# Kernel optimization log

Hardware: AMD Instinct MI355X
Metric: run time of the kernel (lower is better)

Reference implementation:

```python
import jax, jax.numpy as jnp
import numpy as np

D_MODEL, H, DH = 1024, 16, 64
S, B, LCACHE = 16, 8, 8192
W_SCALE = 0.02  # keep pre-softmax logits in a sane range


def setup_inputs() -> dict:
    key = jax.random.key(0)
    ks = jax.random.split(key, 7)
    return {
        "x": jax.random.normal(ks[0], (S, B, D_MODEL), jnp.float32),
        "cache_k": jax.random.normal(ks[1], (LCACHE, B, H, DH), jnp.float32),
        "cache_v": jax.random.normal(ks[2], (LCACHE, B, H, DH), jnp.float32),
        "Wq": jax.random.normal(ks[3], (D_MODEL, H * DH), jnp.float32) * W_SCALE,
        "Wk": jax.random.normal(ks[4], (D_MODEL, H * DH), jnp.float32) * W_SCALE,
        "Wv": jax.random.normal(ks[5], (D_MODEL, H * DH), jnp.float32) * W_SCALE,
        "Wo": jax.random.normal(ks[6], (H * DH, D_MODEL), jnp.float32) * W_SCALE,
    }


def reference(x, cache_k, cache_v, Wq, Wk, Wv, Wo):
    S, B, D = x.shape
    Lc, _, H, Dh = cache_k.shape
    # project and split heads: (S, B, H, Dh)
    q = (x @ Wq).reshape(S, B, H, Dh)
    k_new = (x @ Wk).reshape(S, B, H, Dh)
    v_new = (x @ Wv).reshape(S, B, H, Dh)
    # extend cache along time axis -> (L, B, H, Dh), L = Lc + S
    new_k = jnp.concatenate([cache_k, k_new], axis=0)
    new_v = jnp.concatenate([cache_v, v_new], axis=0)
    L = Lc + S
    scale = 1.0 / jnp.sqrt(jnp.asarray(Dh, x.dtype))
    # scores: (B, H, S, L)
    scores = jnp.einsum('sbhd,tbhd->bhst', q, new_k) * scale
    # causal: query at position Lc+s attends to key positions t <= Lc+s
    mask = jnp.arange(L)[None, :] <= (Lc + jnp.arange(S))[:, None]  # (S, L)
    scores = jnp.where(mask[None, None], scores, jnp.asarray(-1e9, scores.dtype))
    attn = jax.nn.softmax(scores, axis=-1)
    ctx = jnp.einsum('bhst,tbhd->sbhd', attn, new_v).reshape(S, B, H * Dh)
    res = ctx @ Wo  # (S, B, D)
    return res, new_k, new_v
```

## Files before the change

### kernel.cpp

```cpp
#include <hip/hip_runtime.h>
#include <hip/hip_bf16.h>

#define S 16
#define B 8
#define H 16
#define DH 64
#define D 1024
#define HD 1024
#define LC 8192
#define LMAX (LC + S)
#define NCH 32
#define CHT 256
#define TILE 32
#define NT (CHT / TILE)

typedef __attribute__((ext_vector_type(4))) float f4;
typedef __attribute__((ext_vector_type(4))) short s4v;
typedef __attribute__((ext_vector_type(8))) short s8v;

__device__ inline short bfs(float f) {
    __hip_bfloat16 h = __float2bfloat16(f);
    return __builtin_bit_cast(short, h);
}
__device__ inline s4v pack4(float a, float b, float c, float d) {
    s4v r; r[0] = bfs(a); r[1] = bfs(b); r[2] = bfs(c); r[3] = bfs(d); return r;
}

__global__ __launch_bounds__(256) void proj_qkv(const float* __restrict__ x,
        const float* __restrict__ Wq, const float* __restrict__ Wk,
        const float* __restrict__ Wv,
        float* __restrict__ q_ws, float* __restrict__ newk, float* __restrict__ newv)
{
    int bx = blockIdx.x;
    int rg  = bx / 12;
    int rem = bx % 12;
    int mat = rem >> 2, chunk = rem & 3;
    int o = chunk * 256 + threadIdx.x;
    const float* W  = (mat == 0) ? Wq : ((mat == 1) ? Wk : Wv);
    const float* xr = x + (size_t)rg * 4 * D;

    float a0 = 0.f, a1 = 0.f, a2 = 0.f, a3 = 0.f;
    #pragma unroll 16
    for (int d = 0; d < D; ++d) {
        float w = W[(size_t)d * HD + o];
        a0 += xr[d] * w;
        a1 += xr[D + d] * w;
        a2 += xr[2 * D + d] * w;
        a3 += xr[3 * D + d] * w;
    }
    float acc[4] = {a0, a1, a2, a3};
    #pragma unroll
    for (int i = 0; i < 4; ++i) {
        int row = rg * 4 + i;
        int s = row >> 3, b = row & 7;
        if (mat == 0) {
            q_ws[(size_t)row * HD + o] = acc[i];
        } else {
            float* dst = (mat == 1) ? newk : newv;
            dst[(size_t)((LC + s) * B + b) * HD + o] = acc[i];
        }
    }
}

__global__ __launch_bounds__(256) void attn_fused(const float* __restrict__ q_ws,
        const float* __restrict__ cache_k, const float* __restrict__ cache_v,
        float* __restrict__ newk, float* __restrict__ newv,
        float* __restrict__ m_part, float* __restrict__ l_part,
        float* __restrict__ pv_part)
{
    extern __shared__ char smem[];
    short* Ksp = (short*)smem;
    short* Vp  = Ksp + TILE * 256;

    int bx = blockIdx.x;
    int chunk = bx & 31;
    int hgb = bx >> 5;
    int hg = hgb & 3, b = hgb >> 2;
    int tid = threadIdx.x, l = tid & 63, wid = tid >> 6;
    int g = l >> 4, c16 = l & 15;
    int h = hg * 4 + wid;
    unsigned vbase = (unsigned)(uintptr_t)Vp + (unsigned)wid * 4160u;

    s8v qf[2];
    {
        const float* qp = q_ws + ((size_t)(c16 * B + b)) * HD + h * DH + g * 8;
        #pragma unroll
        for (int sl = 0; sl < 2; ++sl) {
            float4 qa = *(const float4*)(qp + sl * 32);
            float4 qb = *(const float4*)(qp + sl * 32 + 4);
            s8v q;
            q[0] = bfs(qa.x * 0.125f); q[1] = bfs(qa.y * 0.125f);
            q[2] = bfs(qa.z * 0.125f); q[3] = bfs(qa.w * 0.125f);
            q[4] = bfs(qb.x * 0.125f); q[5] = bfs(qb.y * 0.125f);
            q[6] = bfs(qb.z * 0.125f); q[7] = bfs(qb.w * 0.125f);
            qf[sl] = q;
        }
    }

    float m_prev = -1e30f, l_acc = 0.f;
    f4 acc[4] = {{0,0,0,0},{0,0,0,0},{0,0,0,0},{0,0,0,0}};

    int t0base = chunk * CHT;
    int sw = (c16 & 7) << 3;

    for (int it = 0; it < NT; ++it) {
        int t0 = t0base + it * TILE;
        asm volatile("s_waitcnt lgkmcnt(0)" ::: "memory");
        __builtin_amdgcn_s_barrier();
        __builtin_amdgcn_sched_barrier(0);

        #pragma unroll
        for (int gg = 0; gg < 8; ++gg) {
            int idx = tid + gg * 256;
            int rr = idx >> 6, ch = idx & 63;
            size_t off = ((size_t)(t0 + rr)) * 8192 + (size_t)b * 1024 + hg * 256 + ch * 4;
            f4 k4 = __builtin_nontemporal_load((const f4*)(cache_k + off));
            f4 v4 = __builtin_nontemporal_load((const f4*)(cache_v + off));
            __builtin_nontemporal_store(k4, (f4*)(newk + off));
            __builtin_nontemporal_store(v4, (f4*)(newv + off));
            int w = ch >> 4, cc = ch & 15;
            int kidx = rr * 256 + w * 64 + ((cc * 4) ^ ((rr & 7) << 3));
            *(s4v*)(Ksp + kidx) = pack4(k4[0], k4[1], k4[2], k4[3]);
            int vidx = w * 2080 + (cc >> 2) * 520 + (rr >> 2) * 64 + (rr & 3) * 16 + (cc & 3) * 4;
            *(s4v*)(Vp + vidx) = pack4(v4[0], v4[1], v4[2], v4[3]);
        }
        asm volatile("s_waitcnt lgkmcnt(0)" ::: "memory");
        __builtin_amdgcn_s_barrier();
        __builtin_amdgcn_sched_barrier(0);

        f4 d0 = {0,0,0,0}, d1 = {0,0,0,0};
        #pragma unroll
        for (int sl = 0; sl < 2; ++sl) {
            int col = (sl * 32 + g * 8) ^ sw;
            s8v k0 = *(const s8v*)(Ksp + c16 * 256 + wid * 64 + col);
            s8v k1 = *(const s8v*)(Ksp + (16 + c16) * 256 + wid * 64 + col);
            d0 = __builtin_amdgcn_mfma_f32_16x16x32_bf16(k0, qf[sl], d0, 0, 0, 0);
            d1 = __builtin_amdgcn_mfma_f32_16x16x32_bf16(k1, qf[sl], d1, 0, 0, 0);
        }
        float hm = fmaxf(fmaxf(fmaxf(d0[0], d0[1]), fmaxf(d0[2], d0[3])),
                         fmaxf(fmaxf(d1[0], d1[1]), fmaxf(d1[2], d1[3])));
        hm = fmaxf(hm, __shfl_xor(hm, 16));
        hm = fmaxf(hm, __shfl_xor(hm, 32));
        float mn = fmaxf(m_prev, hm);
        float sf = __expf(m_prev - mn);
        m_prev = mn;
        f4 p0, p1;
        #pragma unroll
        for (int r = 0; r < 4; ++r) { p0[r] = __expf(d0[r] - mn); p1[r] = __expf(d1[r] - mn); }
        float rs = (p0[0] + p0[1] + p0[2] + p0[3]) + (p1[0] + p1[1] + p1[2] + p1[3]);
        rs += __shfl_xor(rs, 16);
        rs += __shfl_xor(rs, 32);
        l_acc = l_acc * sf + rs;
        #pragma unroll
        for (int dd = 0; dd < 4; ++dd) acc[dd] *= sf;

        s4v pb0 = pack4(p0[0], p0[1], p0[2], p0[3]);
        s4v pb1 = pack4(p1[0], p1[1], p1[2], p1[3]);
        s4v vfr[4][2];
        #pragma unroll
        for (int dd = 0; dd < 4; ++dd) {
            #pragma unroll
            for (int hh = 0; hh < 2; ++hh) {
                unsigned adr = vbase + 2u * (unsigned)(dd * 520 + (hh * 4 + g) * 64 + c16);
                asm volatile("ds_read_b64_tr_b16 %0, %1" : "=v"(vfr[dd][hh]) : "v"(adr));
            }
        }
        asm volatile("s_waitcnt lgkmcnt(0)" ::: "memory");
        __builtin_amdgcn_sched_barrier(0);
        #pragma unroll
        for (int dd = 0; dd < 4; ++dd) {
            acc[dd] = __builtin_amdgcn_mfma_f32_16x16x16bf16_1k(vfr[dd][0], pb0, acc[dd], 0, 0, 0);
            acc[dd] = __builtin_amdgcn_mfma_f32_16x16x16bf16_1k(vfr[dd][1], pb1, acc[dd], 0, 0, 0);
        }
    }

    if (chunk == NCH - 1) {
        __syncthreads();
        #pragma unroll
        for (int q = 0; q < 4; ++q) {
            int idx = tid + q * 256;
            int rr = idx >> 6, ch = idx & 63;
            size_t off = ((size_t)(LC + rr)) * 8192 + (size_t)b * 1024 + hg * 256 + ch * 4;
            float4 k4 = *(const float4*)(newk + off);
            float4 v4 = *(const float4*)(newv + off);
            int w = ch >> 4, cc = ch & 15;
            int kidx = rr * 256 + w * 64 + ((cc * 4) ^ ((rr & 7) << 3));
            *(s4v*)(Ksp + kidx) = pack4(k4.x, k4.y, k4.z, k4.w);
            int vidx = w * 2080 + (cc >> 2) * 520 + (rr >> 2) * 64 + (rr & 3) * 16 + (cc & 3) * 4;
            *(s4v*)(Vp + vidx) = pack4(v4.x, v4.y, v4.z, v4.w);
        }
        __syncthreads();
        f4 d0 = {0,0,0,0};
        #pragma unroll
        for (int sl = 0; sl < 2; ++sl) {
            int col = (sl * 32 + g * 8) ^ sw;
            s8v k0 = *(const s8v*)(Ksp + c16 * 256 + wid * 64 + col);
            d0 = __builtin_amdgcn_mfma_f32_16x16x32_bf16(k0, qf[sl], d0, 0, 0, 0);
        }
        #pragma unroll
        for (int r = 0; r < 4; ++r)
            if (4 * g + r > c16) d0[r] = -1e30f;
        float hm = fmaxf(fmaxf(d0[0], d0[1]), fmaxf(d0[2], d0[3]));
        hm = fmaxf(hm, __shfl_xor(hm, 16));
        hm = fmaxf(hm, __shfl_xor(hm, 32));
        float mn = fmaxf(m_prev, hm);
        float sf = __expf(m_prev - mn);
        m_prev = mn;
        f4 p0;
        #pragma unroll
        for (int r = 0; r < 4; ++r) p0[r] = __expf(d0[r] - mn);
        float rs = (p0[0] + p0[1]) + (p0[2] + p0[3]);
        rs += __shfl_xor(rs, 16);
        rs += __shfl_xor(rs, 32);
        l_acc = l_acc * sf + rs;
        #pragma unroll
        for (int dd = 0; dd < 4; ++dd) acc[dd] *= sf;
        s4v pb0 = pack4(p0[0], p0[1], p0[2], p0[3]);
        s4v vfr[4];
        #pragma unroll
        for (int dd = 0; dd < 4; ++dd) {
            unsigned adr = vbase + 2u * (unsigned)(dd * 520 + g * 64 + c16);
            asm volatile("ds_read_b64_tr_b16 %0, %1" : "=v"(vfr[dd]) : "v"(adr));
        }
        asm volatile("s_waitcnt lgkmcnt(0)" ::: "memory");
        __builtin_amdgcn_sched_barrier(0);
        #pragma unroll
        for (int dd = 0; dd < 4; ++dd)
            acc[dd] = __builtin_amdgcn_mfma_f32_16x16x16bf16_1k(vfr[dd], pb0, acc[dd], 0, 0, 0);
    }

    int pi = ((b * 16 + h) * NCH) + chunk;
    #pragma unroll
    for (int dd = 0; dd < 4; ++dd)
        #pragma unroll
        for (int r = 0; r < 4; ++r)
            pv_part[((size_t)pi * 64 + dd * 16 + g * 4 + r) * 16 + c16] = acc[dd][r];
    if (l < 16) {
        m_part[pi * 16 + l] = m_prev;
        l_part[pi * 16 + l] = l_acc;
    }
}

__global__ __launch_bounds__(256) void combine(const float* __restrict__ m_part,
        const float* __restrict__ l_part, const float* __restrict__ pv_part,
        float* __restrict__ ctx)
{
    __shared__ float wexp[NCH][16];
    __shared__ float Ls[16];
    int bh = blockIdx.x;
    int h = bh & 15, b = bh >> 4;
    int tid = threadIdx.x;
    if (tid < 16) {
        int s = tid;
        float M = -1e30f;
        #pragma unroll
        for (int c = 0; c < NCH; ++c) M = fmaxf(M, m_part[(bh * NCH + c) * 16 + s]);
        float L = 0.f;
        #pragma unroll
        for (int c = 0; c < NCH; ++c) {
            float e = __expf(m_part[(bh * NCH + c) * 16 + s] - M);
            wexp[c][s] = e;
            L += e * l_part[(bh * NCH + c) * 16 + s];
        }
        Ls[s] = L;
    }
    __syncthreads();
    #pragma unroll
    for (int k = 0; k < 4; ++k) {
        int idx = tid + k * 256;
        int d = idx >> 4, s = idx & 15;
        float v = 0.f;
        #pragma unroll
        for (int c = 0; c < NCH; ++c)
            v += wexp[c][s] * pv_part[((size_t)(bh * NCH + c) * 64 + d) * 16 + s];
        ctx[((size_t)(s * B + b)) * HD + h * DH + d] = v / Ls[s];
    }
}

__global__ __launch_bounds__(256) void proj_o(const float* __restrict__ ctx,
                                              const float* __restrict__ Wo,
                                              float* __restrict__ res)
{
    int bx = blockIdx.x;
    int rg = bx >> 2, chunk = bx & 3;
    int o = chunk * 256 + threadIdx.x;
    const float* cr = ctx + (size_t)rg * 4 * HD;

    float a0 = 0.f, a1 = 0.f, a2 = 0.f, a3 = 0.f;
    #pragma unroll 16
    for (int d = 0; d < HD; ++d) {
        float w = Wo[(size_t)d * D + o];
        a0 += cr[d] * w;
        a1 += cr[HD + d] * w;
        a2 += cr[2 * HD + d] * w;
        a3 += cr[3 * HD + d] * w;
    }
    res[(size_t)(rg * 4 + 0) * D + o] = a0;
    res[(size_t)(rg * 4 + 1) * D + o] = a1;
    res[(size_t)(rg * 4 + 2) * D + o] = a2;
    res[(size_t)(rg * 4 + 3) * D + o] = a3;
}

extern "C" void kernel_launch(void* const* d_in, const int* in_sizes, int n_in,
                              void* d_out, int out_size, void* d_ws, size_t ws_size,
                              hipStream_t stream)
{
    const float* x  = (const float*)d_in[0];
    const float* ck = (const float*)d_in[1];
    const float* cv = (const float*)d_in[2];
    const float* Wq = (const float*)d_in[3];
    const float* Wk = (const float*)d_in[4];
    const float* Wv = (const float*)d_in[5];
    const float* Wo = (const float*)d_in[6];

    float* out  = (float*)d_out;
    float* res  = out;
    float* newk = out + (size_t)S * B * D;
    float* newv = newk + (size_t)LMAX * B * H * DH;

    float* q_ws    = (float*)d_ws;
    float* ctx     = q_ws + (size_t)S * B * HD;
    float* m_part  = ctx + (size_t)S * B * HD;
    float* l_part  = m_part + (size_t)B * H * NCH * S;
    float* pv_part = l_part + (size_t)B * H * NCH * S;

    size_t smem = (size_t)TILE * 256 * 2 + 4 * 2080 * 2;

    hipLaunchKernelGGL(proj_qkv, dim3(32 * 12), dim3(256), 0, stream,
                       x, Wq, Wk, Wv, q_ws, newk, newv);
    hipLaunchKernelGGL(attn_fused, dim3(B * 4 * NCH), dim3(256), smem, stream,
                       q_ws, ck, cv, newk, newv, m_part, l_part, pv_part);
    hipLaunchKernelGGL(combine, dim3(B * H), dim3(256), 0, stream,
                       m_part, l_part, pv_part, ctx);
    hipLaunchKernelGGL(proj_o, dim3(32 * 4), dim3(256), 0, stream,
                       ctx, Wo, res);
}
```

Before: 358.7 us.

## Register double-buffer KV cache loads and fuse combine with output projection

The attention kernel now prefetches the next tile of K/V cache into registers while the current tile is written to the output cache and staged to LDS. The tile shrinks to 16 rows to keep the register footprint small, and launch bounds request higher occupancy. The combine and Wo-projection kernels are merged: each block applies its head's slice of Wo and atomically accumulates into a result that proj_qkv zero-initialises, removing one launch and the ctx round-trip. Atomic adds make the summation order nondeterministic, and the smaller tiles mean more barriers per chunk.

Result: faster. 295.4 us (-17.6%).

```diff
diff --git a/kernel.cpp b/kernel.cpp
--- a/kernel.cpp
+++ b/kernel.cpp
@@ -11,7 +11,7 @@
 #define LMAX (LC + S)
 #define NCH 32
 #define CHT 256
-#define TILE 32
+#define TILE 16
 #define NT (CHT / TILE)
 
 typedef __attribute__((ext_vector_type(4))) float f4;
@@ -29,7 +29,8 @@
 __global__ __launch_bounds__(256) void proj_qkv(const float* __restrict__ x,
         const float* __restrict__ Wq, const float* __restrict__ Wk,
         const float* __restrict__ Wv,
-        float* __restrict__ q_ws, float* __restrict__ newk, float* __restrict__ newv)
+        float* __restrict__ q_ws, float* __restrict__ newk, float* __restrict__ newv,
+        float* __restrict__ res)
 {
     int bx = blockIdx.x;
     int rg  = bx / 12;
@@ -55,6 +56,7 @@
         int s = row >> 3, b = row & 7;
         if (mat == 0) {
             q_ws[(size_t)row * HD + o] = acc[i];
+            res[(size_t)row * D + o] = 0.f;
         } else {
             float* dst = (mat == 1) ? newk : newv;
             dst[(size_t)((LC + s) * B + b) * HD + o] = acc[i];
@@ -62,7 +64,7 @@
     }
 }
 
-__global__ __launch_bounds__(256) void attn_fused(const float* __restrict__ q_ws,
+__global__ __launch_bounds__(256, 4) void attn_fused(const float* __restrict__ q_ws,
         const float* __restrict__ cache_k, const float* __restrict__ cache_v,
         float* __restrict__ newk, float* __restrict__ newv,
         float* __restrict__ m_part, float* __restrict__ l_part,
@@ -79,7 +81,9 @@
     int tid = threadIdx.x, l = tid & 63, wid = tid >> 6;
     int g = l >> 4, c16 = l & 15;
     int h = hg * 4 + wid;
-    unsigned vbase = (unsigned)(uintptr_t)Vp + (unsigned)wid * 4160u;
+    int rrb = tid >> 6, ch = tid & 63;
+    int w = ch >> 4, cc = ch & 15;
+    unsigned vbase = (unsigned)(uintptr_t)Vp + (unsigned)wid * 2112u;
 
     s8v qf[2];
     {
@@ -102,52 +106,65 @@
 
     int t0base = chunk * CHT;
     int sw = (c16 & 7) << 3;
-
+    size_t cbase = (size_t)b * 1024 + hg * 256 + ch * 4;
+
+    f4 kb[2][4], vb[2][4];
+    #pragma unroll
+    for (int gg = 0; gg < 4; ++gg) {
+        size_t off = ((size_t)(t0base + rrb + 4 * gg)) * 8192 + cbase;
+        kb[0][gg] = __builtin_nontemporal_load((const f4*)(cache_k + off));
+        vb[0][gg] = __builtin_nontemporal_load((const f4*)(cache_v + off));
+    }
+
+    #pragma unroll
     for (int it = 0; it < NT; ++it) {
+        const int cur = it & 1, nxt = cur ^ 1;
         int t0 = t0base + it * TILE;
+
+        if (it + 1 < NT) {
+            #pragma unroll
+            for (int gg = 0; gg < 4; ++gg) {
+                size_t off = ((size_t)(t0 + TILE + rrb + 4 * gg)) * 8192 + cbase;
+                kb[nxt][gg] = __builtin_nontemporal_load((const f4*)(cache_k + off));
+                vb[nxt][gg] = __builtin_nontemporal_load((const f4*)(cache_v + off));
+            }
+        }
         asm volatile("s_waitcnt lgkmcnt(0)" ::: "memory");
         __builtin_amdgcn_s_barrier();
         __builtin_amdgcn_sched_barrier(0);
 
         #pragma unroll
-        for (int gg = 0; gg < 8; ++gg) {
-            int idx = tid + gg * 256;
-            int rr = idx >> 6, ch = idx & 63;
-            size_t off = ((size_t)(t0 + rr)) * 8192 + (size_t)b * 1024 + hg * 256 + ch * 4;
-            f4 k4 = __builtin_nontemporal_load((const f4*)(cache_k + off));
-            f4 v4 = __builtin_nontemporal_load((const f4*)(cache_v + off));
-            __builtin_nontemporal_store(k4, (f4*)(newk + off));
-            __builtin_nontemporal_store(v4, (f4*)(newv + off));
-            int w = ch >> 4, cc = ch & 15;
+        for (int gg = 0; gg < 4; ++gg) {
+            int rr = rrb + 4 * gg;
+            size_t off = ((size_t)(t0 + rr)) * 8192 + cbase;
+            __builtin_nontemporal_store(kb[cur][gg], (f4*)(newk + off));
+            __builtin_nontemporal_store(vb[cur][gg], (f4*)(newv + off));
             int kidx = rr * 256 + w * 64 + ((cc * 4) ^ ((rr & 7) << 3));
-            *(s4v*)(Ksp + kidx) = pack4(k4[0], k4[1], k4[2], k4[3]);
-            int vidx = w * 2080 + (cc >> 2) * 520 + (rr >> 2) * 64 + (rr & 3) * 16 + (cc & 3) * 4;
-            *(s4v*)(Vp + vidx) = pack4(v4[0], v4[1], v4[2], v4[3]);
+            *(s4v*)(Ksp + kidx) = pack4(kb[cur][gg][0], kb[cur][gg][1], kb[cur][gg][2], kb[cur][gg][3]);
+            int vidx = w * 1056 + (cc >> 2) * 264 + (rr >> 2) * 64 + (rr & 3) * 16 + (cc & 3) * 4;
+            *(s4v*)(Vp + vidx) = pack4(vb[cur][gg][0], vb[cur][gg][1], vb[cur][gg][2], vb[cur][gg][3]);
         }
         asm volatile("s_waitcnt lgkmcnt(0)" ::: "memory");
         __builtin_amdgcn_s_barrier();
         __builtin_amdgcn_sched_barrier(0);
 
-        f4 d0 = {0,0,0,0}, d1 = {0,0,0,0};
+        f4 d0 = {0,0,0,0};
         #pragma unroll
         for (int sl = 0; sl < 2; ++sl) {
             int col = (sl * 32 + g * 8) ^ sw;
             s8v k0 = *(const s8v*)(Ksp + c16 * 256 + wid * 64 + col);
-            s8v k1 = *(const s8v*)(Ksp + (16 + c16) * 256 + wid * 64 + col);
             d0 = __builtin_amdgcn_mfma_f32_16x16x32_bf16(k0, qf[sl], d0, 0, 0, 0);
-            d1 = __builtin_amdgcn_mfma_f32_16x16x32_bf16(k1, qf[sl], d1, 0, 0, 0);
-        }
-        float hm = fmaxf(fmaxf(fmaxf(d0[0], d0[1]), fmaxf(d0[2], d0[3])),
-                         fmaxf(fmaxf(d1[0], d1[1]), fmaxf(d1[2], d1[3])));
+        }
+        float hm = fmaxf(fmaxf(d0[0], d0[1]), fmaxf(d0[2], d0[3]));
         hm = fmaxf(hm, __shfl_xor(hm, 16));
         hm = fmaxf(hm, __shfl_xor(hm, 32));
         float mn = fmaxf(m_prev, hm);
         float sf = __expf(m_prev - mn);
         m_prev = mn;
-        f4 p0, p1;
-        #pragma unroll
-        for (int r = 0; r < 4; ++r) { p0[r] = __expf(d0[r] - mn); p1[r] = __expf(d1[r] - mn); }
-        float rs = (p0[0] + p0[1] + p0[2] + p0[3]) + (p1[0] + p1[1] + p1[2] + p1[3]);
+        f4 p0;
+        #pragma unroll
+        for (int r = 0; r < 4; ++r) p0[r] = __expf(d0[r] - mn);
+        float rs = (p0[0] + p0[1]) + (p0[2] + p0[3]);
         rs += __shfl_xor(rs, 16);
         rs += __shfl_xor(rs, 32);
         l_acc = l_acc * sf + rs;
@@ -155,23 +172,17 @@
         for (int dd = 0; dd < 4; ++dd) acc[dd] *= sf;
 
         s4v pb0 = pack4(p0[0], p0[1], p0[2], p0[3]);
-        s4v pb1 = pack4(p1[0], p1[1], p1[2], p1[3]);
-        s4v vfr[4][2];
+        s4v vfr[4];
         #pragma unroll
         for (int dd = 0; dd < 4; ++dd) {
-            #pragma unroll
-            for (int hh = 0; hh < 2; ++hh) {
-                unsigned adr = vbase + 2u * (unsigned)(dd * 520 + (hh * 4 + g) * 64 + c16);
-                asm volatile("ds_read_b64_tr_b16 %0, %1" : "=v"(vfr[dd][hh]) : "v"(adr));
-            }
+            unsigned adr = vbase + 2u * (unsigned)(dd * 264 + g * 64 + c16);
+            asm volatile("ds_read_b64_tr_b16 %0, %1" : "=v"(vfr[dd]) : "v"(adr));
         }
         asm volatile("s_waitcnt lgkmcnt(0)" ::: "memory");
         __builtin_amdgcn_sched_barrier(0);
         #pragma unroll
-        for (int dd = 0; dd < 4; ++dd) {
-            acc[dd] = __builtin_amdgcn_mfma_f32_16x16x16bf16_1k(vfr[dd][0], pb0, acc[dd], 0, 0, 0);
-            acc[dd] = __builtin_amdgcn_mfma_f32_16x16x16bf16_1k(vfr[dd][1], pb1, acc[dd], 0, 0, 0);
-        }
+        for (int dd = 0; dd < 4; ++dd)
+            acc[dd] = __builtin_amdgcn_mfma_f32_16x16x16bf16_1k(vfr[dd], pb0, acc[dd], 0, 0, 0);
     }
 
     if (chunk == NCH - 1) {
@@ -179,14 +190,14 @@
         #pragma unroll
         for (int q = 0; q < 4; ++q) {
             int idx = tid + q * 256;
-            int rr = idx >> 6, ch = idx & 63;
-            size_t off = ((size_t)(LC + rr)) * 8192 + (size_t)b * 1024 + hg * 256 + ch * 4;
+            int rr = idx >> 6, c2 = idx & 63;
+            int w2 = c2 >> 4, cc2 = c2 & 15;
+            size_t off = ((size_t)(LC + rr)) * 8192 + (size_t)b * 1024 + hg * 256 + c2 * 4;
             float4 k4 = *(const float4*)(newk + off);
             float4 v4 = *(const float4*)(newv + off);
-            int w = ch >> 4, cc = ch & 15;
-            int kidx = rr * 256 + w * 64 + ((cc * 4) ^ ((rr & 7) << 3));
+            int kidx = rr * 256 + w2 * 64 + ((cc2 * 4) ^ ((rr & 7) << 3));
             *(s4v*)(Ksp + kidx) = pack4(k4.x, k4.y, k4.z, k4.w);
-            int vidx = w * 2080 + (cc >> 2) * 520 + (rr >> 2) * 64 + (rr & 3) * 16 + (cc & 3) * 4;
+            int vidx = w2 * 1056 + (cc2 >> 2) * 264 + (rr >> 2) * 64 + (rr & 3) * 16 + (cc2 & 3) * 4;
             *(s4v*)(Vp + vidx) = pack4(v4.x, v4.y, v4.z, v4.w);
         }
         __syncthreads();
@@ -219,7 +230,7 @@
         s4v vfr[4];
         #pragma unroll
         for (int dd = 0; dd < 4; ++dd) {
-            unsigned adr = vbase + 2u * (unsigned)(dd * 520 + g * 64 + c16);
+            unsigned adr = vbase + 2u * (unsigned)(dd * 264 + g * 64 + c16);
             asm volatile("ds_read_b64_tr_b16 %0, %1" : "=v"(vfr[dd]) : "v"(adr));
         }
         asm volatile("s_waitcnt lgkmcnt(0)" ::: "memory");
@@ -241,15 +252,18 @@
     }
 }
 
-__global__ __launch_bounds__(256) void combine(const float* __restrict__ m_part,
+__global__ __launch_bounds__(256) void combine_proj(const float* __restrict__ m_part,
         const float* __restrict__ l_part, const float* __restrict__ pv_part,
-        float* __restrict__ ctx)
+        const float* __restrict__ Wo, float* __restrict__ res)
 {
     __shared__ float wexp[NCH][16];
     __shared__ float Ls[16];
-    int bh = blockIdx.x;
+    __shared__ float cds[64][16];
+    int bx = blockIdx.x;
+    int oc = bx & 3, bh = bx >> 2;
     int h = bh & 15, b = bh >> 4;
     int tid = threadIdx.x;
+
     if (tid < 16) {
         int s = tid;
         float M = -1e30f;
@@ -273,32 +287,29 @@
         #pragma unroll
         for (int c = 0; c < NCH; ++c)
             v += wexp[c][s] * pv_part[((size_t)(bh * NCH + c) * 64 + d) * 16 + s];
-        ctx[((size_t)(s * B + b)) * HD + h * DH + d] = v / Ls[s];
-    }
-}
-
-__global__ __launch_bounds__(256) void proj_o(const float* __restrict__ ctx,
-                                              const float* __restrict__ Wo,
-                                              float* __restrict__ res)
-{
-    int bx = blockIdx.x;
-    int rg = bx >> 2, chunk = bx & 3;
-    int o = chunk * 256 + threadIdx.x;
-    const float* cr = ctx + (size_t)rg * 4 * HD;
-
-    float a0 = 0.f, a1 = 0.f, a2 = 0.f, a3 = 0.f;
-    #pragma unroll 16
-    for (int d = 0; d < HD; ++d) {
-        float w = Wo[(size_t)d * D + o];
-        a0 += cr[d] * w;
-        a1 += cr[HD + d] * w;
-        a2 += cr[2 * HD + d] * w;
-        a3 += cr[3 * HD + d] * w;
-    }
-    res[(size_t)(rg * 4 + 0) * D + o] = a0;
-    res[(size_t)(rg * 4 + 1) * D + o] = a1;
-    res[(size_t)(rg * 4 + 2) * D + o] = a2;
-    res[(size_t)(rg * 4 + 3) * D + o] = a3;
+        cds[d][s] = v / Ls[s];
+    }
+    __syncthreads();
+
+    int o = oc * 256 + tid;
+    float acc[16];
+    #pragma unroll
+    for (int s = 0; s < 16; ++s) acc[s] = 0.f;
+    #pragma unroll 8
+    for (int d = 0; d < 64; ++d) {
+        float wv = Wo[(size_t)(h * 64 + d) * D + o];
+        #pragma unroll
+        for (int q = 0; q < 4; ++q) {
+            f4 cq = *(const f4*)&cds[d][q * 4];
+            acc[q * 4 + 0] += cq[0] * wv;
+            acc[q * 4 + 1] += cq[1] * wv;
+            acc[q * 4 + 2] += cq[2] * wv;
+            acc[q * 4 + 3] += cq[3] * wv;
+        }
+    }
+    #pragma unroll
+    for (int s = 0; s < 16; ++s)
+        atomicAdd(res + (size_t)(s * B + b) * D + o, acc[s]);
 }
 
 extern "C" void kernel_launch(void* const* d_in, const int* in_sizes, int n_in,
@@ -324,14 +335,12 @@
     float* l_part  = m_part + (size_t)B * H * NCH * S;
     float* pv_part = l_part + (size_t)B * H * NCH * S;
 
-    size_t smem = (size_t)TILE * 256 * 2 + 4 * 2080 * 2;
+    size_t smem = (size_t)(TILE * 256 + 4 * 1056) * 2;
 
     hipLaunchKernelGGL(proj_qkv, dim3(32 * 12), dim3(256), 0, stream,
-                       x, Wq, Wk, Wv, q_ws, newk, newv);
+                       x, Wq, Wk, Wv, q_ws, newk, newv, res);
     hipLaunchKernelGGL(attn_fused, dim3(B * 4 * NCH), dim3(256), smem, stream,
                        q_ws, ck, cv, newk, newv, m_part, l_part, pv_part);
-    hipLaunchKernelGGL(combine, dim3(B * H), dim3(256), 0, stream,
-                       m_part, l_part, pv_part, ctx);
-    hipLaunchKernelGGL(proj_o, dim3(32 * 4), dim3(256), 0, stream,
-                       ctx, Wo, res);
-}
+    hipLaunchKernelGGL(combine_proj, dim3(B * H * 4), dim3(256), 0, stream,
+                       m_part, l_part, pv_part, Wo, res);
+}
```
